# Kernel optimization log

Measured on AMD Instinct MI355X. Metric: run time of the kernel, lower is better.

Reference implementation:

```python
import jax, jax.numpy as jnp
import numpy as np

B, T, D, H = 2, 4096, 768, 12
HD = D // H  # head_dim = 64


def setup_inputs() -> dict:
    key = jax.random.key(0)
    ks = jax.random.split(key, 6)
    s = 0.02
    return {
        "x": jax.random.normal(ks[0], (B, T, D), dtype=jnp.float32),
        "Wq": jax.random.normal(ks[1], (D, D), dtype=jnp.float32) * s,
        "Wk": jax.random.normal(ks[2], (D, D), dtype=jnp.float32) * s,
        "Wv": jax.random.normal(ks[3], (D, D), dtype=jnp.float32) * s,
        "Wo": jax.random.normal(ks[4], (D, D), dtype=jnp.float32) * s,
        "bo": jnp.zeros((D,), dtype=jnp.float32),
    }


def reference(x, Wq, Wk, Wv, Wo, bo):
    b, t, d = x.shape
    # QKV projections (no bias), reshape to [B, H, T, HD]
    def heads(w):
        return (x @ w.T).reshape(b, t, H, HD).transpose(0, 2, 1, 3)
    q, k, v = heads(Wq), heads(Wk), heads(Wv)
    scores = jnp.einsum("bhqd,bhkd->bhqk", q, k)  # [B,H,T,T]
    causal = jnp.tril(jnp.ones((t, t), dtype=bool))
    scores = jnp.where(causal, scores, -jnp.inf)
    attn = jax.nn.softmax(scores / jnp.sqrt(jnp.float32(HD)), axis=-1)
    ctx = jnp.einsum("bhqk,bhkd->bhqd", attn, v)  # [B,H,T,HD]
    ctx = ctx.transpose(0, 2, 1, 3).reshape(b, t, d)
    return ctx @ Wo.T + bo
```

## Files before the change

kernel.cpp:

```cpp
#include <hip/hip_runtime.h>
#include <hip/hip_bf16.h>
#include <cstdint>
#include <cstddef>

#define B_  2
#define T_  4096
#define D_  768
#define H_  12
#define HD_ 64
#define M_  (B_*T_)

#define SCL 0.18033688f

typedef __bf16 bf16x8 __attribute__((ext_vector_type(8)));
typedef float  f32x4  __attribute__((ext_vector_type(4)));
typedef short  s16x4  __attribute__((ext_vector_type(4)));
using bf16 = __hip_bfloat16;

__device__ inline float fexp2(float x) {
  float r; asm("v_exp_f32 %0, %1" : "=v"(r) : "v"(x)); return r;
}
__device__ inline uint32_t fu(float x) { union { float f; uint32_t u; } c; c.f = x; return c.u; }
__device__ inline uint32_t pktr(float a, float b) {
  return __builtin_amdgcn_perm(fu(b), fu(a), 0x07060302);
}
__device__ inline f32x4 mfma16(s16x4 a, s16x4 b, f32x4 c) {
#if __has_builtin(__builtin_amdgcn_mfma_f32_16x16x16bf16_1k)
  return __builtin_amdgcn_mfma_f32_16x16x16bf16_1k(a, b, c, 0, 0, 0);
#else
  asm("v_mfma_f32_16x16x16_bf16 %0, %1, %2, %0" : "+v"(c) : "v"(a), "v"(b));
  return c;
#endif
}
#define GLD16(g, l) __builtin_amdgcn_global_load_lds( \
    (const __attribute__((address_space(1))) uint32_t*)(const void*)(g), \
    (__attribute__((address_space(3))) uint32_t*)(void*)(l), 16, 0, 0)

__global__ void cvt_all(const float* __restrict__ x,
                        const float* __restrict__ w0, const float* __restrict__ w1,
                        const float* __restrict__ w2, const float* __restrict__ w3,
                        bf16* __restrict__ xd,
                        bf16* __restrict__ d0, bf16* __restrict__ d1,
                        bf16* __restrict__ d2, bf16* __restrict__ d3) {
  int blk = blockIdx.x;
  const float* s; bf16* d; int i;
  if (blk < 6144) {
    s = x; d = xd; i = blk * 256 + threadIdx.x;
  } else {
    int q = blk - 6144, which = q / 576, rb = q % 576;
    switch (which) {
      case 0: s = w0; d = d0; break;
      case 1: s = w1; d = d1; break;
      case 2: s = w2; d = d2; break;
      default: s = w3; d = d3; break;
    }
    i = rb * 256 + threadIdx.x;
  }
  float4 v = ((const float4*)s)[i];
  union { bf16 o[4]; uint2 u; } pk;
  pk.o[0] = __float2bfloat16(v.x); pk.o[1] = __float2bfloat16(v.y);
  pk.o[2] = __float2bfloat16(v.z); pk.o[3] = __float2bfloat16(v.w);
  *(uint2*)(d + 4 * (size_t)i) = pk.u;
}

__global__ __launch_bounds__(256) void gemm_qkv(const bf16* __restrict__ x,
                                                const bf16* __restrict__ W0,
                                                const bf16* __restrict__ W1,
                                                const bf16* __restrict__ W2,
                                                bf16* __restrict__ O0,
                                                bf16* __restrict__ O1,
                                                bf16* __restrict__ O2t) {
  __shared__ bf16 As[2][4096];
  __shared__ bf16 Bs[2][4096];
  const int flat = blockIdx.x;
  const int by = flat / 18;
  const int rr = flat % 18;
  const int z  = rr / 6;
  const int bx = rr % 6;
  const bf16* Wz = (z == 0) ? W0 : ((z == 1) ? W1 : W2);
  const char* Ap; const char* Bp; int a0, b0;
  if (z == 2) { Ap = (const char*)x;  a0 = by * 128; Bp = (const char*)Wz; b0 = bx * 128; }
  else        { Ap = (const char*)Wz; a0 = bx * 128; Bp = (const char*)x;  b0 = by * 128; }
  const int t = threadIdx.x;
  const int w = t >> 6, lane = t & 63;
  const int wa = (w >> 1) * 64, wb = (w & 1) * 64;
  const int mi = lane & 15, qd = lane >> 4;

  int aoff[2], boff[2];
  #pragma unroll
  for (int i = 0; i < 2; ++i) {
    int L = i * 256 + t;
    int row = L >> 2, sl = L & 3, c = sl ^ (row & 3);
    aoff[i] = (a0 + row) * 1536 + c * 16;
    boff[i] = (b0 + row) * 1536 + c * 16;
  }
  const int fsw = (qd ^ (mi & 3)) * 8;

  f32x4 acc[4][4] = {};

  #pragma unroll
  for (int i = 0; i < 2; ++i) {
    GLD16(Ap + aoff[i], &As[0][i * 2048 + w * 512]);
    GLD16(Bp + boff[i], &Bs[0][i * 2048 + w * 512]);
  }

  for (int kk = 0; kk < 24; ++kk) {
    __syncthreads();
    const int par = kk & 1;
    if (kk + 1 < 24) {
      const int np = par ^ 1, kb = (kk + 1) * 64;
      #pragma unroll
      for (int i = 0; i < 2; ++i) {
        GLD16(Ap + aoff[i] + kb, &As[np][i * 2048 + w * 512]);
        GLD16(Bp + boff[i] + kb, &Bs[np][i * 2048 + w * 512]);
      }
    }
    bf16x8 af[4], bfr[4];
    #pragma unroll
    for (int at = 0; at < 4; ++at)
      af[at] = *(const bf16x8*)&As[par][(wa + at * 16 + mi) * 32 + fsw];
    #pragma unroll
    for (int bt = 0; bt < 4; ++bt)
      bfr[bt] = *(const bf16x8*)&Bs[par][(wb + bt * 16 + mi) * 32 + fsw];
    #pragma unroll
    for (int at = 0; at < 4; ++at)
      #pragma unroll
      for (int bt = 0; bt < 4; ++bt)
        acc[at][bt] = __builtin_amdgcn_mfma_f32_16x16x32_bf16(af[at], bfr[bt], acc[at][bt], 0, 0, 0);
  }

  if (z == 2) {
    #pragma unroll
    for (int at = 0; at < 4; ++at)
      #pragma unroll
      for (int bt = 0; bt < 4; ++bt) {
        int gr = a0 + wa + at * 16 + qd * 4;
        int gc = b0 + wb + bt * 16 + mi;
        union { bf16 o[4]; uint2 u; } pk;
        #pragma unroll
        for (int r = 0; r < 4; ++r) pk.o[r] = __float2bfloat16(acc[at][bt][r]);
        int bb = gr >> 12, tt = gr & 4095;
        int ttw = tt ^ (((gc >> 3) & 1) << 2);
        *(uint2*)(O2t + (size_t)bb * 768 * 4096 + (size_t)gc * 4096 + ttw) = pk.u;
      }
  } else {
    const float scl = (z == 1) ? SCL : 1.0f;
    bf16* Ob = (z == 0) ? O0 : O1;
    #pragma unroll
    for (int at = 0; at < 4; ++at)
      #pragma unroll
      for (int bt = 0; bt < 4; ++bt) {
        int f0  = a0 + wa + at * 16 + qd * 4;
        int tkn = b0 + wb + bt * 16 + mi;
        union { bf16 o[4]; uint2 u; } pk;
        #pragma unroll
        for (int r = 0; r < 4; ++r) pk.o[r] = __float2bfloat16(acc[at][bt][r] * scl);
        *(uint2*)(Ob + (size_t)tkn * 768 + f0) = pk.u;
      }
  }
}

__global__ __launch_bounds__(256) void gemm_out(const bf16* __restrict__ ctx,
                                                const bf16* __restrict__ Wo,
                                                float* __restrict__ Cf,
                                                const float* __restrict__ bias) {
  __shared__ bf16 As[2][2048];
  __shared__ bf16 Bs[2][4096];
  const int flat = blockIdx.x;
  const int by = flat / 12, bx = flat % 12;
  const char* Ap = (const char*)Wo;  const int a0 = bx * 64;
  const char* Bp = (const char*)ctx; const int b0 = by * 128;
  const int t = threadIdx.x;
  const int w = t >> 6, lane = t & 63;
  const int wa = (w >> 1) * 32, wb = (w & 1) * 64;
  const int mi = lane & 15, qd = lane >> 4;

  int aoff, boff[2];
  { int row = t >> 2, sl = t & 3, c = sl ^ (row & 3);
    aoff = (a0 + row) * 1536 + c * 16; }
  #pragma unroll
  for (int i = 0; i < 2; ++i) {
    int L = i * 256 + t;
    int row = L >> 2, sl = L & 3, c = sl ^ (row & 3);
    boff[i] = (b0 + row) * 1536 + c * 16;
  }
  const int fsw = (qd ^ (mi & 3)) * 8;

  f32x4 acc[2][4] = {};

  GLD16(Ap + aoff, &As[0][w * 512]);
  #pragma unroll
  for (int i = 0; i < 2; ++i)
    GLD16(Bp + boff[i], &Bs[0][i * 2048 + w * 512]);

  for (int kk = 0; kk < 24; ++kk) {
    __syncthreads();
    const int par = kk & 1;
    if (kk + 1 < 24) {
      const int np = par ^ 1, kb = (kk + 1) * 64;
      GLD16(Ap + aoff + kb, &As[np][w * 512]);
      #pragma unroll
      for (int i = 0; i < 2; ++i)
        GLD16(Bp + boff[i] + kb, &Bs[np][i * 2048 + w * 512]);
    }
    bf16x8 af[2], bfr[4];
    #pragma unroll
    for (int at = 0; at < 2; ++at)
      af[at] = *(const bf16x8*)&As[par][(wa + at * 16 + mi) * 32 + fsw];
    #pragma unroll
    for (int bt = 0; bt < 4; ++bt)
      bfr[bt] = *(const bf16x8*)&Bs[par][(wb + bt * 16 + mi) * 32 + fsw];
    #pragma unroll
    for (int at = 0; at < 2; ++at)
      #pragma unroll
      for (int bt = 0; bt < 4; ++bt)
        acc[at][bt] = __builtin_amdgcn_mfma_f32_16x16x32_bf16(af[at], bfr[bt], acc[at][bt], 0, 0, 0);
  }

  #pragma unroll
  for (int at = 0; at < 2; ++at)
    #pragma unroll
    for (int bt = 0; bt < 4; ++bt) {
      int f0  = a0 + wa + at * 16 + qd * 4;
      int tkn = b0 + wb + bt * 16 + mi;
      float4 bv = *(const float4*)&bias[f0];
      float4 o;
      o.x = acc[at][bt][0] + bv.x; o.y = acc[at][bt][1] + bv.y;
      o.z = acc[at][bt][2] + bv.z; o.w = acc[at][bt][3] + bv.w;
      *(float4*)&Cf[(size_t)tkn * 768 + f0] = o;
    }
}

__global__ __launch_bounds__(256, 3) void flash_attn(const bf16* __restrict__ Q,
                                                     const bf16* __restrict__ K,
                                                     const bf16* __restrict__ Vt,
                                                     bf16* __restrict__ ctx) {
  __shared__ bf16 Ks[2][4096];
  __shared__ bf16 Vs[2][4096];
  const int t = threadIdx.x;
  const int w = t >> 6, lane = t & 63;
  const int mi = lane & 15, qd = lane >> 4;
  const int bh   = blockIdx.x % 24;
  const int qrev = blockIdx.x / 24;
  const int q0 = T_ - 128 - qrev * 128;
  const int b = bh / H_, h = bh % H_;
  const size_t bTD = (size_t)b * T_ * D_;
  const char* Kp = (const char*)(K  + bTD + (size_t)h * HD_);
  const char* Vp = (const char*)(Vt + (size_t)b * D_ * T_ + (size_t)h * HD_ * T_);
  const int qw = q0 + w * 32;

  int vkoff[2], vvoff[2];
  #pragma unroll
  for (int i = 0; i < 2; ++i) {
    int L = i * 256 + t;
    int rl = L >> 3, c = (L & 7) ^ (rl & 7);
    vkoff[i] = rl * 1536 + c * 16;
    vvoff[i] = rl * 8192 + c * 16;
  }

  int fidx[4][2];
  #pragma unroll
  for (int jt = 0; jt < 4; ++jt)
    #pragma unroll
    for (int kt = 0; kt < 2; ++kt)
      fidx[jt][kt] = (jt * 16 + mi) * 64 + (((kt * 4 + qd) ^ (mi & 7)) * 8);

  int vbase[4];
  #pragma unroll
  for (int ks = 0; ks < 4; ++ks)
    vbase[ks] = (((2 * ks + (qd >> 1)) ^ (mi & 7)) * 8) +
                (((qd & 1) ^ ((mi >> 3) & 1)) * 4) + mi * 64;

  bf16x8 qf[2][2];
  const bf16* Qp = Q + bTD + (size_t)h * HD_;
  #pragma unroll
  for (int s = 0; s < 2; ++s)
    #pragma unroll
    for (int kt = 0; kt < 2; ++kt)
      qf[s][kt] = *(const bf16x8*)(Qp + (size_t)(qw + s * 16 + mi) * D_ + kt * 32 + qd * 8);

  f32x4 oacc[2][4] = {};
  float lst[2] = {0.f, 0.f};
  const int ntiles = q0 / 64 + 2;

  #pragma unroll
  for (int i = 0; i < 2; ++i) {
    GLD16(Kp + vkoff[i], &Ks[0][i * 2048 + w * 512]);
    GLD16(Vp + vvoff[i], &Vs[0][i * 2048 + w * 512]);
  }

  for (int tt = 0; tt < ntiles; ++tt) {
    __syncthreads();
    const int par = tt & 1;
    if (tt + 1 < ntiles) {
      const size_t j1 = (size_t)(tt + 1) * 64;
      const int np = par ^ 1;
      #pragma unroll
      for (int i = 0; i < 2; ++i) {
        GLD16(Kp + vkoff[i] + j1 * 1536, &Ks[np][i * 2048 + w * 512]);
        GLD16(Vp + vvoff[i] + j1 * 2,    &Vs[np][i * 2048 + w * 512]);
      }
    }
    const int j0 = tt * 64;
    if (j0 > qw + 31) continue;

    f32x4 sacc[2][4] = {};
    __builtin_amdgcn_s_setprio(1);
    #pragma unroll
    for (int jt = 0; jt < 4; ++jt)
      #pragma unroll
      for (int kt = 0; kt < 2; ++kt) {
        bf16x8 kf = *(const bf16x8*)&Ks[par][fidx[jt][kt]];
        sacc[0][jt] = __builtin_amdgcn_mfma_f32_16x16x32_bf16(kf, qf[0][kt], sacc[0][jt], 0, 0, 0);
        sacc[1][jt] = __builtin_amdgcn_mfma_f32_16x16x32_bf16(kf, qf[1][kt], sacc[1][jt], 0, 0, 0);
      }
    __builtin_amdgcn_s_setprio(0);

    if (j0 + 63 > qw) {
      #pragma unroll
      for (int s = 0; s < 2; ++s) {
        const int qg = qw + s * 16 + mi;
        #pragma unroll
        for (int jt = 0; jt < 4; ++jt)
          #pragma unroll
          for (int r = 0; r < 4; ++r) {
            int jg = j0 + jt * 16 + qd * 4 + r;
            if (jg > qg) sacc[s][jt][r] = -1e30f;
          }
      }
    }

    s16x4 pB[2][4];
    #pragma unroll
    for (int s = 0; s < 2; ++s)
      #pragma unroll
      for (int jt = 0; jt < 4; ++jt) {
        float p0 = fexp2(sacc[s][jt][0]);
        float p1 = fexp2(sacc[s][jt][1]);
        float p2 = fexp2(sacc[s][jt][2]);
        float p3 = fexp2(sacc[s][jt][3]);
        lst[s] += (p0 + p1) + (p2 + p3);
        union { uint32_t u[2]; s16x4 v; } pw;
        pw.u[0] = pktr(p0, p1);
        pw.u[1] = pktr(p2, p3);
        pB[s][jt] = pw.v;
      }

    __builtin_amdgcn_s_setprio(1);
    #pragma unroll
    for (int ks = 0; ks < 4; ++ks)
      #pragma unroll
      for (int dt = 0; dt < 4; ++dt) {
        s16x4 vf = *(const s16x4*)&Vs[par][vbase[ks] + dt * 1024];
        oacc[0][dt] = mfma16(vf, pB[0][ks], oacc[0][dt]);
        oacc[1][dt] = mfma16(vf, pB[1][ks], oacc[1][dt]);
      }
    __builtin_amdgcn_s_setprio(0);
  }

  #pragma unroll
  for (int s = 0; s < 2; ++s) {
    float l = lst[s];
    l += __shfl_xor(l, 16);
    l += __shfl_xor(l, 32);
    float inv = __builtin_amdgcn_rcpf(l);
    const int qg = qw + s * 16 + mi;
    bf16* cp = ctx + bTD + (size_t)qg * D_ + h * HD_ + qd * 4;
    #pragma unroll
    for (int dt = 0; dt < 4; ++dt) {
      union { bf16 o[4]; uint2 u; } pko;
      #pragma unroll
      for (int r = 0; r < 4; ++r) pko.o[r] = __float2bfloat16(oacc[s][dt][r] * inv);
      *(uint2*)(cp + dt * 16) = pko.u;
    }
  }
}

extern "C" void kernel_launch(void* const* d_in, const int* in_sizes, int n_in,
                              void* d_out, int out_size, void* d_ws, size_t ws_size,
                              hipStream_t stream) {
  const float* x  = (const float*)d_in[0];
  const float* Wq = (const float*)d_in[1];
  const float* Wk = (const float*)d_in[2];
  const float* Wv = (const float*)d_in[3];
  const float* Wo = (const float*)d_in[4];
  const float* bo = (const float*)d_in[5];
  float* out = (float*)d_out;

  char* ws = (char*)d_ws;
  const size_t SZ  = (size_t)M_ * D_ * 2;
  const size_t WSZ = (size_t)D_ * D_ * 2;
  bf16* xb   = (bf16*)(ws);
  bf16* Qb   = (bf16*)(ws + 1 * SZ);
  bf16* Kb   = (bf16*)(ws + 2 * SZ);
  bf16* Vtg  = (bf16*)(ws + 3 * SZ);
  bf16* ctxb = (bf16*)(ws + 4 * SZ);
  bf16* Wqb  = (bf16*)(ws + 5 * SZ);
  bf16* Wkb  = (bf16*)(ws + 5 * SZ + 1 * WSZ);
  bf16* Wvb  = (bf16*)(ws + 5 * SZ + 2 * WSZ);
  bf16* Wob  = (bf16*)(ws + 5 * SZ + 3 * WSZ);

  cvt_all<<<6144 + 4 * 576, 256, 0, stream>>>(x, Wq, Wk, Wv, Wo, xb, Wqb, Wkb, Wvb, Wob);

  gemm_qkv<<<1152, 256, 0, stream>>>(xb, Wqb, Wkb, Wvb, Qb, Kb, Vtg);

  flash_attn<<<(T_ / 128) * B_ * H_, 256, 0, stream>>>(Qb, Kb, Vtg, ctxb);

  gemm_out<<<768, 256, 0, stream>>>(ctxb, Wob, out, bo);
}
```

Baseline: 254.7 us.

## Use 16x16x32 MFMA for PV with permuted K rows, 64-query blocks

The P·V product now uses the 16x16x32 bf16 MFMA with bf16x8 operands instead of the 16x16x16 variant. K rows are loaded in a permuted order so the score accumulator layout matches the B operand of the wider MFMA, which lets V be read with the same swizzled indexing as K. The V-transpose swizzle in the QKV GEMM is dropped to match. Attention blocks shrink from 256 to 128 threads covering 64 queries, doubling the grid. The per-warp causal skip is removed, so each block now processes all its tiles.

```diff
diff --git a/kernel.cpp b/kernel.cpp
--- a/kernel.cpp
+++ b/kernel.cpp
@@ -14,7 +14,6 @@
 
 typedef __bf16 bf16x8 __attribute__((ext_vector_type(8)));
 typedef float  f32x4  __attribute__((ext_vector_type(4)));
-typedef short  s16x4  __attribute__((ext_vector_type(4)));
 using bf16 = __hip_bfloat16;
 
 __device__ inline float fexp2(float x) {
@@ -23,14 +22,6 @@
 __device__ inline uint32_t fu(float x) { union { float f; uint32_t u; } c; c.f = x; return c.u; }
 __device__ inline uint32_t pktr(float a, float b) {
   return __builtin_amdgcn_perm(fu(b), fu(a), 0x07060302);
-}
-__device__ inline f32x4 mfma16(s16x4 a, s16x4 b, f32x4 c) {
-#if __has_builtin(__builtin_amdgcn_mfma_f32_16x16x16bf16_1k)
-  return __builtin_amdgcn_mfma_f32_16x16x16bf16_1k(a, b, c, 0, 0, 0);
-#else
-  asm("v_mfma_f32_16x16x16_bf16 %0, %1, %2, %0" : "+v"(c) : "v"(a), "v"(b));
-  return c;
-#endif
 }
 #define GLD16(g, l) __builtin_amdgcn_global_load_lds( \
     (const __attribute__((address_space(1))) uint32_t*)(const void*)(g), \
@@ -140,8 +131,7 @@
         #pragma unroll
         for (int r = 0; r < 4; ++r) pk.o[r] = __float2bfloat16(acc[at][bt][r]);
         int bb = gr >> 12, tt = gr & 4095;
-        int ttw = tt ^ (((gc >> 3) & 1) << 2);
-        *(uint2*)(O2t + (size_t)bb * 768 * 4096 + (size_t)gc * 4096 + ttw) = pk.u;
+        *(uint2*)(O2t + (size_t)bb * 768 * 4096 + (size_t)gc * 4096 + tt) = pk.u;
       }
   } else {
     const float scl = (z == 1) ? SCL : 1.0f;
@@ -231,7 +221,7 @@
     }
 }
 
-__global__ __launch_bounds__(256, 3) void flash_attn(const bf16* __restrict__ Q,
+__global__ __launch_bounds__(128, 2) void flash_attn(const bf16* __restrict__ Q,
                                                      const bf16* __restrict__ K,
                                                      const bf16* __restrict__ Vt,
                                                      bf16* __restrict__ ctx) {
@@ -242,19 +232,20 @@
   const int mi = lane & 15, qd = lane >> 4;
   const int bh   = blockIdx.x % 24;
   const int qrev = blockIdx.x / 24;
-  const int q0 = T_ - 128 - qrev * 128;
+  const int q0 = T_ - 64 - qrev * 64;
   const int b = bh / H_, h = bh % H_;
   const size_t bTD = (size_t)b * T_ * D_;
   const char* Kp = (const char*)(K  + bTD + (size_t)h * HD_);
   const char* Vp = (const char*)(Vt + (size_t)b * D_ * T_ + (size_t)h * HD_ * T_);
   const int qw = q0 + w * 32;
 
-  int vkoff[2], vvoff[2];
-  #pragma unroll
-  for (int i = 0; i < 2; ++i) {
-    int L = i * 256 + t;
+  int vkoff[4], vvoff[4];
+  #pragma unroll
+  for (int i = 0; i < 4; ++i) {
+    int L = i * 128 + t;
     int rl = L >> 3, c = (L & 7) ^ (rl & 7);
-    vkoff[i] = rl * 1536 + c * 16;
+    int jrow = (rl & 32) | ((rl & 0xC) << 1) | ((rl & 16) >> 2) | (rl & 3);
+    vkoff[i] = jrow * 1536 + c * 16;
     vvoff[i] = rl * 8192 + c * 16;
   }
 
@@ -265,12 +256,6 @@
     for (int kt = 0; kt < 2; ++kt)
       fidx[jt][kt] = (jt * 16 + mi) * 64 + (((kt * 4 + qd) ^ (mi & 7)) * 8);
 
-  int vbase[4];
-  #pragma unroll
-  for (int ks = 0; ks < 4; ++ks)
-    vbase[ks] = (((2 * ks + (qd >> 1)) ^ (mi & 7)) * 8) +
-                (((qd & 1) ^ ((mi >> 3) & 1)) * 4) + mi * 64;
-
   bf16x8 qf[2][2];
   const bf16* Qp = Q + bTD + (size_t)h * HD_;
   #pragma unroll
@@ -281,12 +266,12 @@
 
   f32x4 oacc[2][4] = {};
   float lst[2] = {0.f, 0.f};
-  const int ntiles = q0 / 64 + 2;
-
-  #pragma unroll
-  for (int i = 0; i < 2; ++i) {
-    GLD16(Kp + vkoff[i], &Ks[0][i * 2048 + w * 512]);
-    GLD16(Vp + vvoff[i], &Vs[0][i * 2048 + w * 512]);
+  const int ntiles = q0 / 64 + 1;
+
+  #pragma unroll
+  for (int i = 0; i < 4; ++i) {
+    GLD16(Kp + vkoff[i], &Ks[0][i * 1024 + w * 512]);
+    GLD16(Vp + vvoff[i], &Vs[0][i * 1024 + w * 512]);
   }
 
   for (int tt = 0; tt < ntiles; ++tt) {
@@ -296,13 +281,12 @@
       const size_t j1 = (size_t)(tt + 1) * 64;
       const int np = par ^ 1;
       #pragma unroll
-      for (int i = 0; i < 2; ++i) {
-        GLD16(Kp + vkoff[i] + j1 * 1536, &Ks[np][i * 2048 + w * 512]);
-        GLD16(Vp + vvoff[i] + j1 * 2,    &Vs[np][i * 2048 + w * 512]);
+      for (int i = 0; i < 4; ++i) {
+        GLD16(Kp + vkoff[i] + j1 * 1536, &Ks[np][i * 1024 + w * 512]);
+        GLD16(Vp + vvoff[i] + j1 * 2,    &Vs[np][i * 1024 + w * 512]);
       }
     }
     const int j0 = tt * 64;
-    if (j0 > qw + 31) continue;
 
     f32x4 sacc[2][4] = {};
     __builtin_amdgcn_s_setprio(1);
@@ -324,15 +308,16 @@
         for (int jt = 0; jt < 4; ++jt)
           #pragma unroll
           for (int r = 0; r < 4; ++r) {
-            int jg = j0 + jt * 16 + qd * 4 + r;
+            int jg = j0 + ((jt >> 1) << 5) + (qd << 3) + ((jt & 1) << 2) + r;
             if (jg > qg) sacc[s][jt][r] = -1e30f;
           }
       }
     }
 
-    s16x4 pB[2][4];
-    #pragma unroll
-    for (int s = 0; s < 2; ++s)
+    bf16x8 pB[2][2];
+    #pragma unroll
+    for (int s = 0; s < 2; ++s) {
+      uint32_t pu[4][2];
       #pragma unroll
       for (int jt = 0; jt < 4; ++jt) {
         float p0 = fexp2(sacc[s][jt][0]);
@@ -340,20 +325,26 @@
         float p2 = fexp2(sacc[s][jt][2]);
         float p3 = fexp2(sacc[s][jt][3]);
         lst[s] += (p0 + p1) + (p2 + p3);
-        union { uint32_t u[2]; s16x4 v; } pw;
-        pw.u[0] = pktr(p0, p1);
-        pw.u[1] = pktr(p2, p3);
-        pB[s][jt] = pw.v;
-      }
+        pu[jt][0] = pktr(p0, p1);
+        pu[jt][1] = pktr(p2, p3);
+      }
+      #pragma unroll
+      for (int kt = 0; kt < 2; ++kt) {
+        union { uint32_t u[4]; bf16x8 v; } m;
+        m.u[0] = pu[2 * kt][0];     m.u[1] = pu[2 * kt][1];
+        m.u[2] = pu[2 * kt + 1][0]; m.u[3] = pu[2 * kt + 1][1];
+        pB[s][kt] = m.v;
+      }
+    }
 
     __builtin_amdgcn_s_setprio(1);
     #pragma unroll
-    for (int ks = 0; ks < 4; ++ks)
+    for (int kt = 0; kt < 2; ++kt)
       #pragma unroll
       for (int dt = 0; dt < 4; ++dt) {
-        s16x4 vf = *(const s16x4*)&Vs[par][vbase[ks] + dt * 1024];
-        oacc[0][dt] = mfma16(vf, pB[0][ks], oacc[0][dt]);
-        oacc[1][dt] = mfma16(vf, pB[1][ks], oacc[1][dt]);
+        bf16x8 vf = *(const bf16x8*)&Vs[par][fidx[dt][kt]];
+        oacc[0][dt] = __builtin_amdgcn_mfma_f32_16x16x32_bf16(vf, pB[0][kt], oacc[0][dt], 0, 0, 0);
+        oacc[1][dt] = __builtin_amdgcn_mfma_f32_16x16x32_bf16(vf, pB[1][kt], oacc[1][dt], 0, 0, 0);
       }
     __builtin_amdgcn_s_setprio(0);
   }
@@ -404,7 +395,7 @@
 
   gemm_qkv<<<1152, 256, 0, stream>>>(xb, Wqb, Wkb, Wvb, Qb, Kb, Vtg);
 
-  flash_attn<<<(T_ / 128) * B_ * H_, 256, 0, stream>>>(Qb, Kb, Vtg, ctxb);
+  flash_attn<<<(T_ / 64) * B_ * H_, 128, 0, stream>>>(Qb, Kb, Vtg, ctxb);
 
   gemm_out<<<768, 256, 0, stream>>>(ctxb, Wob, out, bo);
 }
```

Measured after the change: 247.6 us. 1.03x faster.
